# Performance work log

Hardware: AMD Instinct MI355X
Metric: run time of the kernel (lower is better)

Reference implementation:

```python
import jax, jax.numpy as jnp
import numpy as np

IN_CH = 64
EMBED = 128
OUT_CH = 64
NUM_HEADS = 2
HEAD_DIM = EMBED // NUM_HEADS
B, D, H, W = 2, 16, 16, 16
SEQ = D * H * W


def setup_inputs() -> dict:
    key = jax.random.key(0)
    ks = jax.random.split(key, 12)
    s = lambda fan_in: 1.0 / np.sqrt(fan_in)
    return {
        "x": jax.random.normal(ks[0], (B, IN_CH, D, H, W), dtype=jnp.float32),
        "W_cp": jax.random.uniform(ks[1], (EMBED, IN_CH), jnp.float32, -s(IN_CH), s(IN_CH)),
        "b_cp": jax.random.uniform(ks[2], (EMBED,), jnp.float32, -s(IN_CH), s(IN_CH)),
        "W_q": jax.random.uniform(ks[3], (EMBED, EMBED), jnp.float32, -s(EMBED), s(EMBED)),
        "W_k": jax.random.uniform(ks[4], (EMBED, EMBED), jnp.float32, -s(EMBED), s(EMBED)),
        "W_v": jax.random.uniform(ks[5], (EMBED, EMBED), jnp.float32, -s(EMBED), s(EMBED)),
        "W_o": jax.random.uniform(ks[6], (EMBED, EMBED), jnp.float32, -s(EMBED), s(EMBED)),
        "b_o": jax.random.uniform(ks[7], (EMBED,), jnp.float32, -s(EMBED), s(EMBED)),
        "W_out": jax.random.uniform(ks[8], (OUT_CH, EMBED), jnp.float32, -s(EMBED), s(EMBED)),
        "b_out": jax.random.uniform(ks[9], (OUT_CH,), jnp.float32, -s(EMBED), s(EMBED)),
        "pos": jax.random.normal(ks[10], (1, SEQ, EMBED), dtype=jnp.float32) * 0.02,
        "gate": jnp.float32(0.1),
    }


def reference(x, W_cp, b_cp, W_q, W_k, W_v, W_o, b_o, W_out, b_out, pos, gate):
    b, c, d, h, w = x.shape
    seq = d * h * w
    scale = HEAD_DIM ** (-0.5)
    # (B, C, D, H, W) -> (B, S, C)
    xf = jnp.transpose(x, (0, 2, 3, 4, 1)).reshape(b, seq, c)
    xf = xf @ W_cp.T + b_cp + pos  # (B, S, E)
    # QKV projections, split heads: (B, nh, S, hd)
    def heads(t):
        return jnp.transpose(t.reshape(b, seq, NUM_HEADS, HEAD_DIM), (0, 2, 1, 3))
    q = heads(xf @ W_q.T)
    k = heads(xf @ W_k.T)
    v = heads(xf @ W_v.T)
    attn = jax.nn.softmax(jnp.einsum("bnsd,bntd->bnst", q, k) * scale, axis=-1)
    o = jnp.einsum("bnst,bntd->bnsd", attn, v)  # (B, nh, S, hd)
    o = jnp.transpose(o, (0, 2, 1, 3)).reshape(b, seq, EMBED)
    o = o @ W_o.T + b_o
    o = o @ W_out.T + b_out  # (B, S, out)
    out = jnp.transpose(o, (0, 2, 1)).reshape(b, OUT_CH, d, h, w)
    # in_channels == output_dim -> skip is identity (no conv/BN in original)
    return out + gate * x
```

## Files before the change

### kernel.cpp

```cpp
#include <hip/hip_runtime.h>
#include <hip/hip_bf16.h>
#include <cstdint>

typedef unsigned short u16;
typedef __attribute__((ext_vector_type(8))) short short8;
typedef __attribute__((ext_vector_type(8))) float f32x8;
typedef __attribute__((ext_vector_type(4))) float f32x4;

#define MFMA(a, b, c) __builtin_amdgcn_mfma_f32_16x16x32_bf16((a), (b), (c), 0, 0, 0)

#define SEQ 4096
#define KSPLIT 4

static __device__ __forceinline__ float b2f(u16 u) {
    union { float f; uint32_t i; } c; c.i = ((uint32_t)u) << 16; return c.f;
}
static __device__ __forceinline__ u16 f2b(float f) {
    union { float f; uint32_t i; } c; c.f = f;
    uint32_t r = c.i + 0x7FFF + ((c.i >> 16) & 1);
    return (u16)(r >> 16);
}
static __device__ __forceinline__ short8 ld8(const u16* p) {
    return *reinterpret_cast<const short8*>(p);
}
static __device__ __forceinline__ uint32_t pk2(float a, float b) {
    uint32_t r;
    asm("v_cvt_pk_bf16_f32 %0, %1, %2" : "=v"(r) : "v"(a), "v"(b));
    return r;
}
static __device__ __forceinline__ void gld16(const u16* g, u16* l) {
    __builtin_amdgcn_global_load_lds(
        (const __attribute__((address_space(1))) unsigned int*)g,
        (__attribute__((address_space(3))) unsigned int*)l, 16, 0, 0);
}

__global__ void k_prep(const float* __restrict__ Wo, const float* __restrict__ bo,
                       const float* __restrict__ Wout, const float* __restrict__ bout,
                       const float* __restrict__ Wcp, const float* __restrict__ Wq,
                       const float* __restrict__ Wk, const float* __restrict__ Wv,
                       u16* __restrict__ Wc, float* __restrict__ bc,
                       u16* __restrict__ Wcp_b, u16* __restrict__ Wq_b,
                       u16* __restrict__ Wk_b, u16* __restrict__ Wv_b) {
    int idx = blockIdx.x * 256 + threadIdx.x;
    if (idx < 8192) {
        int co = idx >> 7, e = idx & 127;
        float s = 0.f;
        for (int k = 0; k < 128; k++)
            s += Wout[co * 128 + k] * Wo[k * 128 + e];
        Wc[idx] = f2b(s);
    } else if (idx < 8256) {
        int co = idx - 8192;
        float s = bout[co];
        for (int k = 0; k < 128; k++)
            s += bo[k] * Wout[co * 128 + k];
        bc[co] = s;
    } else if (idx < 16448) {
        int i = idx - 8256;  Wcp_b[i] = f2b(Wcp[i]);
    } else if (idx < 32832) {
        int i = idx - 16448; Wq_b[i] = f2b(Wq[i]);
    } else if (idx < 49216) {
        int i = idx - 32832; Wk_b[i] = f2b(Wk[i]);
    } else if (idx < 65600) {
        int i = idx - 49216; Wv_b[i] = f2b(Wv[i]);
    }
}

__global__ __launch_bounds__(256) void k_front(const float* __restrict__ x,
                                               const u16* __restrict__ Wcp,
                                               const float* __restrict__ bcp,
                                               const float* __restrict__ pos,
                                               const u16* __restrict__ Wq,
                                               const u16* __restrict__ Wk,
                                               const u16* __restrict__ Wv,
                                               u16* __restrict__ Q, u16* __restrict__ K,
                                               u16* __restrict__ V) {
    __shared__ __align__(16) u16 xT[32][72];
    __shared__ __align__(16) u16 xfl[32 * 128];
    int blk = blockIdx.x;
    int b = blk >> 7, sb = (blk & 127) * 32;
    int t = threadIdx.x, w = t >> 6, l = t & 63, lc = l & 15, lg = l >> 4;

    {
        int c = t & 63, so = t >> 6;
        const float* src = x + ((size_t)b * 64 + c) * SEQ + sb + so * 8;
        f32x8 a0 = *reinterpret_cast<const f32x8*>(src);
#pragma unroll
        for (int j = 0; j < 8; j++) xT[so * 8 + j][c] = f2b(a0[j]);
    }
    __syncthreads();

    {
        int rt = w >> 1, eh = w & 1;
        short8 af[2];
        af[0] = ld8(&xT[rt * 16 + lc][lg * 8]);
        af[1] = ld8(&xT[rt * 16 + lc][32 + lg * 8]);
#pragma unroll
        for (int et = 0; et < 4; et++) {
            int nt = eh * 4 + et;
            f32x4 acc = {0.f, 0.f, 0.f, 0.f};
#pragma unroll
            for (int ks = 0; ks < 2; ks++) {
                short8 bfr = ld8(Wcp + (nt * 16 + lc) * 64 + ks * 32 + lg * 8);
                acc = MFMA(af[ks], bfr, acc);
            }
            int e = nt * 16 + lc;
            float be = bcp[e];
            int chunk = e >> 3;
#pragma unroll
            for (int r = 0; r < 4; r++) {
                int sl = rt * 16 + lg * 4 + r;
                float v = acc[r] + be + pos[(size_t)(sb + sl) * 128 + e];
                xfl[sl * 128 + ((chunk ^ (sl & 7)) << 3) + (e & 7)] = f2b(v);
            }
        }
    }
    __syncthreads();

    {
        int st = w & 1, hr = w >> 1;
        short8 afq[4];
#pragma unroll
        for (int ks = 0; ks < 4; ks++)
            afq[ks] = ld8(&xfl[(st * 16 + lc) * 128 + (((ks * 4 + lg) ^ (lc & 7)) << 3)]);

        const float qscl = 0.18033688011112042f;
#pragma unroll
        for (int qk = 0; qk < 2; qk++) {
            const u16* W = qk ? Wk : Wq;
            u16* dst = qk ? K : Q;
#pragma unroll
            for (int et = 0; et < 4; et++) {
                int nt = hr * 4 + et;
                f32x4 acc = {0.f, 0.f, 0.f, 0.f};
#pragma unroll
                for (int ks = 0; ks < 4; ks++) {
                    short8 bfr = ld8(W + (nt * 16 + lc) * 128 + ks * 32 + lg * 8);
                    acc = MFMA(afq[ks], bfr, acc);
                }
                int e = nt * 16 + lc, h = e >> 6, d = e & 63;
                float scl = qk ? 1.0f : qscl;
#pragma unroll
                for (int r = 0; r < 4; r++) {
                    int sr = sb + st * 16 + lg * 4 + r;
                    dst[(((size_t)b * 2 + h) * SEQ + sr) * 64 + d] = f2b(acc[r] * scl);
                }
            }
        }
#pragma unroll
        for (int et = 0; et < 4; et++) {
            int nt = hr * 4 + et;
            f32x4 acc = {0.f, 0.f, 0.f, 0.f};
            short8 wv[4];
#pragma unroll
            for (int ks = 0; ks < 4; ks++)
                wv[ks] = ld8(Wv + (nt * 16 + lc) * 128 + ks * 32 + lg * 8);
#pragma unroll
            for (int ks = 0; ks < 4; ks++)
                acc = MFMA(wv[ks], afq[ks], acc);
#pragma unroll
            for (int r = 0; r < 4; r++) {
                int d = nt * 16 + lg * 4 + r, h = d >> 6, dd = d & 63;
                V[((size_t)(b * 2 + h) * 64 + dd) * SEQ + sb + st * 16 + lc] = f2b(acc[r]);
            }
        }
    }
}

__global__ __launch_bounds__(256) void k_attn(const u16* __restrict__ Q,
                                              const u16* __restrict__ K,
                                              const u16* __restrict__ Vg,
                                              u16* __restrict__ Op,
                                              float2* __restrict__ ml) {
    __shared__ __align__(16) u16 Klds[2][4096];
    __shared__ __align__(16) u16 Vlds[2][4096];
    __shared__ __align__(16) u16 Pl[4][16][64];
    int blk = blockIdx.x;
    int split = blk >> 8, bh = (blk >> 6) & 3, qb = (blk & 63) * 64;
    int kbase = split * (SEQ / KSPLIT);
    const u16* Qp = Q + (size_t)bh * SEQ * 64;
    const u16* Kp = K + (size_t)bh * SEQ * 64;
    const u16* Vp = Vg + (size_t)bh * SEQ * 64;
    int t = threadIdx.x, w = t >> 6, l = t & 63, lc = l & 15, lg = l >> 4;
    uint32_t* plw = (uint32_t*)&Pl[w][0][0];

    int swz8 = ((l & 7) ^ ((l >> 3) & 7)) * 8;
    const u16* kSrc = Kp + (size_t)(kbase + w * 16 + (l >> 3)) * 64 + swz8;
    const u16* vSrc = Vp + (size_t)(w * 16 + (l >> 3)) * SEQ + kbase + swz8;

    short8 qa[2];
    qa[0] = ld8(Qp + (size_t)(qb + w * 16 + lc) * 64 + lg * 8);
    qa[1] = ld8(Qp + (size_t)(qb + w * 16 + lc) * 64 + 32 + lg * 8);

    f32x4 oacc[4];
#pragma unroll
    for (int i = 0; i < 4; i++) oacc[i] = (f32x4){0.f, 0.f, 0.f, 0.f};
    float m = -INFINITY, ls = 0.f;

    int c0 = (lg ^ (lc & 7)) * 8;

#define STAGE(buf, tt) do {                                           \
        const u16* ks_ = kSrc + (size_t)(tt) * 4096;                  \
        const u16* vs_ = vSrc + (tt) * 64;                            \
        gld16(ks_,           &Klds[buf][w * 1024]);                   \
        gld16(ks_ + 512,     &Klds[buf][w * 1024 + 512]);             \
        gld16(vs_,           &Vlds[buf][w * 1024]);                   \
        gld16(vs_ + 8 * SEQ, &Vlds[buf][w * 1024 + 512]);             \
    } while (0)

    STAGE(0, 0);
    __syncthreads();

    for (int tt = 0; tt < SEQ / KSPLIT / 64; tt++) {
        int cur = tt & 1;
        if (tt + 1 < SEQ / KSPLIT / 64) STAGE(cur ^ 1, tt + 1);

        const u16* kb = Klds[cur];
        const u16* vb = Vlds[cur];

        f32x4 sc[4];
#pragma unroll
        for (int nt = 0; nt < 4; nt++) {
            sc[nt] = (f32x4){0.f, 0.f, 0.f, 0.f};
            short8 kf0 = ld8(kb + (nt * 16 + lc) * 64 + c0);
            short8 kf1 = ld8(kb + (nt * 16 + lc) * 64 + (c0 ^ 32));
            sc[nt] = MFMA(kf0, qa[0], sc[nt]);
            sc[nt] = MFMA(kf1, qa[1], sc[nt]);
        }

        float mx = sc[0][0];
#pragma unroll
        for (int nt = 0; nt < 4; nt++)
#pragma unroll
            for (int r = 0; r < 4; r++) mx = fmaxf(mx, sc[nt][r]);
        mx = fmaxf(mx, __shfl_xor(mx, 16));
        mx = fmaxf(mx, __shfl_xor(mx, 32));

        if (__any(mx - m > 8.f)) {
            float mn = fmaxf(m, mx);
            float corr = exp2f(m - mn);
#pragma unroll
            for (int r = 0; r < 4; r++) {
                float cr = __shfl(corr, lg * 4 + r);
#pragma unroll
                for (int dt = 0; dt < 4; dt++) oacc[dt][r] *= cr;
            }
            ls *= corr;
            m = mn;
        }

        float rs = 0.f;
        uint32_t pk[8];
#pragma unroll
        for (int nt = 0; nt < 4; nt++) {
            float p0 = exp2f(sc[nt][0] - m), p1 = exp2f(sc[nt][1] - m);
            float p2 = exp2f(sc[nt][2] - m), p3 = exp2f(sc[nt][3] - m);
            rs += (p0 + p1) + (p2 + p3);
            pk[nt * 2]     = pk2(p0, p1);
            pk[nt * 2 + 1] = pk2(p2, p3);
        }
        rs += __shfl_xor(rs, 16);
        rs += __shfl_xor(rs, 32);
        ls += rs;

#pragma unroll
        for (int nt = 0; nt < 4; nt++) {
            int base = lc * 32 + (((nt * 2 + (lg >> 1)) ^ (lc & 7)) << 2) + (lg & 1) * 2;
            plw[base]     = pk[nt * 2];
            plw[base + 1] = pk[nt * 2 + 1];
        }

#pragma unroll
        for (int ks = 0; ks < 2; ks++) {
            short8 pa = ld8(&Pl[w][lc][(((ks * 4 + lg) ^ (lc & 7)) << 3)]);
#pragma unroll
            for (int dt = 0; dt < 4; dt++) {
                short8 vf = ld8(vb + (dt * 16 + lc) * 64 + (ks ? (c0 ^ 32) : c0));
                oacc[dt] = MFMA(pa, vf, oacc[dt]);
            }
        }
        __syncthreads();
    }
#undef STAGE

    size_t rowbase = (size_t)(split * 4 + bh) * SEQ + qb + w * 16;
#pragma unroll
    for (int dt = 0; dt < 4; dt++)
#pragma unroll
        for (int r = 0; r < 4; r++)
            Op[(rowbase + lg * 4 + r) * 64 + dt * 16 + lc] = f2b(oacc[dt][r]);
    if (l < 16) {
        float2 v; v.x = m; v.y = ls;
        ml[rowbase + lc] = v;
    }
}

__global__ __launch_bounds__(256) void k_back(const u16* __restrict__ Op,
                                              const float2* __restrict__ ml,
                                              const u16* __restrict__ Wc,
                                              const float* __restrict__ bc,
                                              const float* __restrict__ x,
                                              const float* __restrict__ gate,
                                              float* __restrict__ out) {
    __shared__ __align__(16) u16 Ol[32 * 128];
    int blk = blockIdx.x;
    int b = blk >> 7, sb = (blk & 127) * 32;
    int t = threadIdx.x, w = t >> 6, l = t & 63, lc = l & 15, lg = l >> 4;
    float g = gate[0];

    {
        int sl = t >> 3, ci = t & 7;
        int h = ci >> 2, d0 = (ci & 3) * 16;
        size_t rp0 = ((size_t)(b * 2 + h) << 12) + sb + sl;
        float2 e0 = ml[rp0], e1 = ml[rp0 + 16384], e2 = ml[rp0 + 32768], e3 = ml[rp0 + 49152];
        float ms = fmaxf(fmaxf(e0.x, e1.x), fmaxf(e2.x, e3.x));
        float c0 = exp2f(e0.x - ms), c1 = exp2f(e1.x - ms);
        float c2 = exp2f(e2.x - ms), c3 = exp2f(e3.x - ms);
        float inv = 1.0f / (c0 * e0.y + c1 * e1.y + c2 * e2.y + c3 * e3.y);

        const u16* p0 = Op + rp0 * 64 + d0;
        const u16* p1 = p0 + (size_t)16384 * 64;
        const u16* p2 = p0 + (size_t)32768 * 64;
        const u16* p3 = p0 + (size_t)49152 * 64;
#pragma unroll
        for (int half = 0; half < 2; half++) {
            short8 a0 = ld8(p0 + half * 8), a1 = ld8(p1 + half * 8);
            short8 a2 = ld8(p2 + half * 8), a3 = ld8(p3 + half * 8);
            short8 ov;
#pragma unroll
            for (int e = 0; e < 8; e++) {
                float acc = c0 * b2f((u16)a0[e]) + c1 * b2f((u16)a1[e]) +
                            c2 * b2f((u16)a2[e]) + c3 * b2f((u16)a3[e]);
                ov[e] = (short)f2b(acc * inv);
            }
            int chunk = ci * 2 + half;
            *reinterpret_cast<short8*>(&Ol[sl * 128 + ((chunk ^ (sl & 7)) << 3)]) = ov;
        }
    }
    __syncthreads();

    short8 af[4];
#pragma unroll
    for (int ks = 0; ks < 4; ks++)
        af[ks] = ld8(Wc + (w * 16 + lc) * 128 + ks * 32 + lg * 8);

#pragma unroll
    for (int st = 0; st < 2; st++) {
        f32x4 acc = {0.f, 0.f, 0.f, 0.f};
#pragma unroll
        for (int ks = 0; ks < 4; ks++) {
            short8 bfr = ld8(&Ol[(st * 16 + lc) * 128 + (((ks * 4 + lg) ^ (lc & 7)) << 3)]);
            acc = MFMA(af[ks], bfr, acc);
        }
#pragma unroll
        for (int r = 0; r < 4; r++) {
            int co = w * 16 + lg * 4 + r;
            int s = sb + st * 16 + lc;
            size_t idx = ((size_t)b * 64 + co) * SEQ + s;
            out[idx] = acc[r] + bc[co] + g * x[idx];
        }
    }
}

extern "C" void kernel_launch(void* const* d_in, const int* in_sizes, int n_in,
                              void* d_out, int out_size, void* d_ws, size_t ws_size,
                              hipStream_t stream) {
    const float* x    = (const float*)d_in[0];
    const float* Wcp  = (const float*)d_in[1];
    const float* bcp  = (const float*)d_in[2];
    const float* Wq   = (const float*)d_in[3];
    const float* Wk   = (const float*)d_in[4];
    const float* Wv   = (const float*)d_in[5];
    const float* Wo   = (const float*)d_in[6];
    const float* bo   = (const float*)d_in[7];
    const float* Wout = (const float*)d_in[8];
    const float* bout = (const float*)d_in[9];
    const float* pos  = (const float*)d_in[10];
    const float* gate = (const float*)d_in[11];

    char* ws = (char*)d_ws;
    float2* mlp  = (float2*)(ws);
    u16*    Qb   = (u16*)(ws + (2u << 20));
    u16*    Kb   = (u16*)(ws + (4u << 20));
    u16*    Vt   = (u16*)(ws + (6u << 20));
    u16*    Wc   = (u16*)(ws + (10u << 20));
    float*  bc   = (float*)(ws + (10u << 20) + 16384);
    u16*    Wcp_b = (u16*)(ws + (10u << 20) + 32768);
    u16*    Wq_b  = (u16*)(ws + (10u << 20) + 49152);
    u16*    Wk_b  = (u16*)(ws + (10u << 20) + 81920);
    u16*    Wv_b  = (u16*)(ws + (10u << 20) + 114688);
    u16*    Opb  = (u16*)(ws + (10u << 20) + (512u << 10));
    float* out = (float*)d_out;

    hipLaunchKernelGGL(k_prep, dim3(257), dim3(256), 0, stream,
                       Wo, bo, Wout, bout, Wcp, Wq, Wk, Wv,
                       Wc, bc, Wcp_b, Wq_b, Wk_b, Wv_b);
    hipLaunchKernelGGL(k_front, dim3(256), dim3(256), 0, stream,
                       x, Wcp_b, bcp, pos, Wq_b, Wk_b, Wv_b, Qb, Kb, Vt);
    hipLaunchKernelGGL(k_attn, dim3(256 * KSPLIT), dim3(256), 0, stream, Qb, Kb, Vt, Opb, mlp);
    hipLaunchKernelGGL(k_back, dim3(256), dim3(256), 0, stream, Opb, mlp, Wc, bc, x, gate, out);
}
```

Before: 66.62 us.

## Double key-split count and compute softmax row sums with MFMA

```diff
diff --git a/kernel.cpp b/kernel.cpp
--- a/kernel.cpp
+++ b/kernel.cpp
@@ -10,7 +10,8 @@
 #define MFMA(a, b, c) __builtin_amdgcn_mfma_f32_16x16x32_bf16((a), (b), (c), 0, 0, 0)
 
 #define SEQ 4096
-#define KSPLIT 4
+#define KSPLIT 8
+#define NT (SEQ / KSPLIT / 64)
 
 static __device__ __forceinline__ float b2f(u16 u) {
     union { float f; uint32_t i; } c; c.i = ((uint32_t)u) << 16; return c.f;
@@ -191,10 +192,14 @@
     qa[0] = ld8(Qp + (size_t)(qb + w * 16 + lc) * 64 + lg * 8);
     qa[1] = ld8(Qp + (size_t)(qb + w * 16 + lc) * 64 + 32 + lg * 8);
 
-    f32x4 oacc[4];
+    short8 onesb;
+#pragma unroll
+    for (int i = 0; i < 8; i++) onesb[i] = (short)0x3F80;
+
+    f32x4 oacc[4], lsacc = {0.f, 0.f, 0.f, 0.f};
 #pragma unroll
     for (int i = 0; i < 4; i++) oacc[i] = (f32x4){0.f, 0.f, 0.f, 0.f};
-    float m = -INFINITY, ls = 0.f;
+    float m = -INFINITY;
 
     int c0 = (lg ^ (lc & 7)) * 8;
 
@@ -210,9 +215,10 @@
     STAGE(0, 0);
     __syncthreads();
 
-    for (int tt = 0; tt < SEQ / KSPLIT / 64; tt++) {
+#pragma unroll 2
+    for (int tt = 0; tt < NT; tt++) {
         int cur = tt & 1;
-        if (tt + 1 < SEQ / KSPLIT / 64) STAGE(cur ^ 1, tt + 1);
+        if (tt + 1 < NT) STAGE(cur ^ 1, tt + 1);
 
         const u16* kb = Klds[cur];
         const u16* vb = Vlds[cur];
@@ -227,51 +233,46 @@
             sc[nt] = MFMA(kf1, qa[1], sc[nt]);
         }
 
-        float mx = sc[0][0];
-#pragma unroll
-        for (int nt = 0; nt < 4; nt++)
-#pragma unroll
-            for (int r = 0; r < 4; r++) mx = fmaxf(mx, sc[nt][r]);
-        mx = fmaxf(mx, __shfl_xor(mx, 16));
-        mx = fmaxf(mx, __shfl_xor(mx, 32));
+        float mx = fmaxf(fmaxf(sc[0][0], sc[0][1]), fmaxf(sc[0][2], sc[0][3]));
+#pragma unroll
+        for (int nt = 1; nt < 4; nt++)
+            mx = fmaxf(mx, fmaxf(fmaxf(sc[nt][0], sc[nt][1]),
+                                 fmaxf(sc[nt][2], sc[nt][3])));
 
         if (__any(mx - m > 8.f)) {
-            float mn = fmaxf(m, mx);
+            float mr = fmaxf(mx, __shfl_xor(mx, 16));
+            mr = fmaxf(mr, __shfl_xor(mr, 32));
+            float mn = fmaxf(m, mr);
             float corr = exp2f(m - mn);
 #pragma unroll
             for (int r = 0; r < 4; r++) {
                 float cr = __shfl(corr, lg * 4 + r);
 #pragma unroll
                 for (int dt = 0; dt < 4; dt++) oacc[dt][r] *= cr;
-            }
-            ls *= corr;
+                lsacc[r] *= cr;
+            }
             m = mn;
         }
 
-        float rs = 0.f;
         uint32_t pk[8];
 #pragma unroll
         for (int nt = 0; nt < 4; nt++) {
             float p0 = exp2f(sc[nt][0] - m), p1 = exp2f(sc[nt][1] - m);
             float p2 = exp2f(sc[nt][2] - m), p3 = exp2f(sc[nt][3] - m);
-            rs += (p0 + p1) + (p2 + p3);
             pk[nt * 2]     = pk2(p0, p1);
             pk[nt * 2 + 1] = pk2(p2, p3);
         }
-        rs += __shfl_xor(rs, 16);
-        rs += __shfl_xor(rs, 32);
-        ls += rs;
-
 #pragma unroll
         for (int nt = 0; nt < 4; nt++) {
             int base = lc * 32 + (((nt * 2 + (lg >> 1)) ^ (lc & 7)) << 2) + (lg & 1) * 2;
-            plw[base]     = pk[nt * 2];
-            plw[base + 1] = pk[nt * 2 + 1];
+            uint2 u; u.x = pk[nt * 2]; u.y = pk[nt * 2 + 1];
+            *reinterpret_cast<uint2*>(&plw[base]) = u;
         }
 
 #pragma unroll
         for (int ks = 0; ks < 2; ks++) {
             short8 pa = ld8(&Pl[w][lc][(((ks * 4 + lg) ^ (lc & 7)) << 3)]);
+            lsacc = MFMA(pa, onesb, lsacc);
 #pragma unroll
             for (int dt = 0; dt < 4; dt++) {
                 short8 vf = ld8(vb + (dt * 16 + lc) * 64 + (ks ? (c0 ^ 32) : c0));
@@ -288,9 +289,15 @@
 #pragma unroll
         for (int r = 0; r < 4; r++)
             Op[(rowbase + lg * 4 + r) * 64 + dt * 16 + lc] = f2b(oacc[dt][r]);
-    if (l < 16) {
-        float2 v; v.x = m; v.y = ls;
-        ml[rowbase + lc] = v;
+    float mrow[4];
+#pragma unroll
+    for (int r = 0; r < 4; r++) mrow[r] = __shfl(m, lg * 4 + r);
+    if (lc == 0) {
+#pragma unroll
+        for (int r = 0; r < 4; r++) {
+            float2 v; v.x = mrow[r]; v.y = lsacc[r];
+            ml[rowbase + lg * 4 + r] = v;
+        }
     }
 }
 
@@ -311,27 +318,34 @@
         int sl = t >> 3, ci = t & 7;
         int h = ci >> 2, d0 = (ci & 3) * 16;
         size_t rp0 = ((size_t)(b * 2 + h) << 12) + sb + sl;
-        float2 e0 = ml[rp0], e1 = ml[rp0 + 16384], e2 = ml[rp0 + 32768], e3 = ml[rp0 + 49152];
-        float ms = fmaxf(fmaxf(e0.x, e1.x), fmaxf(e2.x, e3.x));
-        float c0 = exp2f(e0.x - ms), c1 = exp2f(e1.x - ms);
-        float c2 = exp2f(e2.x - ms), c3 = exp2f(e3.x - ms);
-        float inv = 1.0f / (c0 * e0.y + c1 * e1.y + c2 * e2.y + c3 * e3.y);
-
-        const u16* p0 = Op + rp0 * 64 + d0;
-        const u16* p1 = p0 + (size_t)16384 * 64;
-        const u16* p2 = p0 + (size_t)32768 * 64;
-        const u16* p3 = p0 + (size_t)49152 * 64;
+        float2 e[KSPLIT];
+        float ms = -INFINITY;
+#pragma unroll
+        for (int k = 0; k < KSPLIT; k++) {
+            e[k] = ml[rp0 + (size_t)k * 16384];
+            ms = fmaxf(ms, e[k].x);
+        }
+        float den = 0.f, c[KSPLIT];
+#pragma unroll
+        for (int k = 0; k < KSPLIT; k++) {
+            c[k] = exp2f(e[k].x - ms);
+            den += c[k] * e[k].y;
+        }
+        float inv = 1.0f / den;
 #pragma unroll
         for (int half = 0; half < 2; half++) {
-            short8 a0 = ld8(p0 + half * 8), a1 = ld8(p1 + half * 8);
-            short8 a2 = ld8(p2 + half * 8), a3 = ld8(p3 + half * 8);
+            float acc[8];
+#pragma unroll
+            for (int j = 0; j < 8; j++) acc[j] = 0.f;
+#pragma unroll
+            for (int k = 0; k < KSPLIT; k++) {
+                short8 a = ld8(Op + (rp0 + (size_t)k * 16384) * 64 + d0 + half * 8);
+#pragma unroll
+                for (int j = 0; j < 8; j++) acc[j] += c[k] * b2f((u16)a[j]);
+            }
             short8 ov;
 #pragma unroll
-            for (int e = 0; e < 8; e++) {
-                float acc = c0 * b2f((u16)a0[e]) + c1 * b2f((u16)a1[e]) +
-                            c2 * b2f((u16)a2[e]) + c3 * b2f((u16)a3[e]);
-                ov[e] = (short)f2b(acc * inv);
-            }
+            for (int j = 0; j < 8; j++) ov[j] = (short)f2b(acc[j] * inv);
             int chunk = ci * 2 + half;
             *reinterpret_cast<short8*>(&Ol[sl * 128 + ((chunk ^ (sl & 7)) << 3)]) = ov;
         }
```

New measurement: 62.84 us. 5.7% less time.
